# Performance work log

Hardware: AMD Instinct MI355X
Metric: run time of the kernel (lower is better)

## Reference

```python
import jax, jax.numpy as jnp
import numpy as np

N_POINTS = 2_000_000
GRID = 256  # voxel grid resolution (D=H=W), production-scale stand-in for source's 128


def setup_inputs() -> dict:
    key = jax.random.key(0)
    k1, k2, k3 = jax.random.split(key, 3)
    coords = jax.random.uniform(k1, (N_POINTS, 3), dtype=jnp.float32,
                                minval=-0.95, maxval=0.95)
    registration_pred = jax.random.normal(k2, (N_POINTS, 3), dtype=jnp.float32) * 0.02
    registration_gt = jax.random.normal(k3, (N_POINTS, 3), dtype=jnp.float32) * 0.02
    return {"registration_pred": registration_pred,
            "registration_gt": registration_gt,
            "coords": coords}


def _splat(pts, size):
    """Trilinear scatter (adjoint of F.grid_sample, align_corners=False,
    zero padding). pts: [N,3] normalized coords in (x,y,z) order mapping to
    (W,H,D). Splats weight 1 per point. Returns [D,H,W] volume."""
    D = H = W = size
    # grid_sample align_corners=False unnormalization: p = ((g+1)*size - 1)/2
    x = ((pts[:, 0] + 1.0) * W - 1.0) * 0.5
    y = ((pts[:, 1] + 1.0) * H - 1.0) * 0.5
    z = ((pts[:, 2] + 1.0) * D - 1.0) * 0.5
    x0f, y0f, z0f = jnp.floor(x), jnp.floor(y), jnp.floor(z)
    fx, fy, fz = x - x0f, y - y0f, z - z0f  # fractional offsets
    x0, y0, z0 = x0f.astype(jnp.int32), y0f.astype(jnp.int32), z0f.astype(jnp.int32)
    vol = jnp.zeros(D * H * W, dtype=pts.dtype)
    for dz in (0, 1):
        wz = fz if dz else (1.0 - fz)
        for dy in (0, 1):
            wy = fy if dy else (1.0 - fy)
            for dx in (0, 1):
                wx = fx if dx else (1.0 - fx)
                xi, yi, zi = x0 + dx, y0 + dy, z0 + dz
                valid = ((xi >= 0) & (xi < W) & (yi >= 0) & (yi < H)
                         & (zi >= 0) & (zi < D))
                w = jnp.where(valid, wx * wy * wz, 0.0)
                idx = jnp.where(valid, (zi * H + yi) * W + xi, 0)
                vol = vol.at[idx].add(w)
    return vol.reshape(D, H, W)


def reference(registration_pred, registration_gt, coords):
    pred_vol = _splat(coords + registration_pred, GRID)
    gt_vol = _splat(coords + registration_gt, GRID)
    # HuberLoss(reduction='sum', delta=1.0)
    d = pred_vol - gt_vol
    ad = jnp.abs(d)
    return jnp.sum(jnp.where(ad <= 1.0, 0.5 * d * d, ad - 0.5))
```

## Files before the change

kernel.cpp:

```cpp
#include <hip/hip_runtime.h>

#define GRID_RES 256
#define NCELLS 1024
#define NB 1024
#define BCAP 6144
#define CCAP 6144
#define NPT 2

#define W_SCALE 2097152.0f
#define INV_W (1.0f / 2097152.0f)
#define L_SCALE 512.0f
#define INV_L (1.0f / 512.0f)

struct CEv { unsigned pk, xyz; };

__device__ __forceinline__ CEv make_cev(float px, float py, float pz,
                                        unsigned sign) {
    float x = ((px + 1.0f) * (float)GRID_RES - 1.0f) * 0.5f;
    float y = ((py + 1.0f) * (float)GRID_RES - 1.0f) * 0.5f;
    float z = ((pz + 1.0f) * (float)GRID_RES - 1.0f) * 0.5f;
    float xf = floorf(x), yf = floorf(y), zf = floorf(z);
    int x0 = (int)xf, y0 = (int)yf, z0 = (int)zf;
    unsigned qx = (unsigned)((x - xf) * 31.0f + 0.5f);
    unsigned qy = (unsigned)((y - yf) * 31.0f + 0.5f);
    unsigned qz = (unsigned)((z - zf) * 15.0f + 0.5f);
    bool valid = (x0 >= -1) & (x0 <= 255) & (y0 >= -1) & (y0 <= 255) &
                 (z0 >= -1) & (z0 <= 255);
    CEv e;
    e.pk = qx | (qy << 5) | (qz << 10) | (sign << 31);
    e.xyz = valid ? ((unsigned)(x0 + 1) | ((unsigned)(y0 + 1) << 10) |
                     ((unsigned)(z0 + 1) << 20) | (1u << 30))
                  : 0u;
    return e;
}

__device__ __forceinline__ bool ev_flat(const CEv& e, unsigned& cell0,
                                        unsigned& w1base, bool& bx, bool& by,
                                        bool& bz) {
    if (!(e.xyz & (1u << 30))) return false;
    int x0 = (int)(e.xyz & 1023u) - 1;
    int y0 = (int)((e.xyz >> 10) & 1023u) - 1;
    int z0 = (int)((e.xyz >> 20) & 1023u) - 1;
    int xlo = (x0 >= 0) ? (x0 >> 5) : 0;
    int ylo = (y0 >= 0) ? (y0 >> 5) : 0;
    int zlo = (z0 >= 0) ? (z0 >> 4) : 0;
    bx = ((x0 & 31) == 31) & ((unsigned)x0 < 255u);
    by = ((y0 & 31) == 31) & ((unsigned)y0 < 255u);
    bz = ((z0 & 15) == 15) & ((unsigned)z0 < 255u);
    cell0 = ((unsigned)zlo << 6) | ((unsigned)ylo << 3) | (unsigned)xlo;
    unsigned lx0 = (unsigned)(x0 - (xlo << 5) + 1);
    unsigned ly0 = (unsigned)(y0 - (ylo << 5) + 1);
    unsigned lz0 = (unsigned)(z0 - (zlo << 4) + 1);
    w1base = e.pk | (lx0 << 14) | (ly0 << 20) | (lz0 << 26);
    return true;
}

__global__ void init_kernel(unsigned* __restrict__ gCursor,
                            int* __restrict__ lossAcc,
                            unsigned* __restrict__ doneCnt) {
    int t = threadIdx.x;
    gCursor[t] = 0;
    if (t == 0) { lossAcc[0] = 0; doneCnt[0] = 0; }
}

__global__ __launch_bounds__(1024) void bin_kernel(
    const float* __restrict__ pred, const float* __restrict__ gt,
    const float* __restrict__ coords, unsigned* __restrict__ gCursor,
    unsigned* __restrict__ payload, int n) {
    __shared__ unsigned h[NCELLS];
    __shared__ unsigned gAdj[NCELLS];
    __shared__ unsigned short itemCell[BCAP];
    __shared__ unsigned wtot[16];
    __shared__ unsigned totalS;
    __shared__ unsigned pl[BCAP];
    int b = blockIdx.x;
    int t = threadIdx.x;
    h[t] = 0;
    __syncthreads();

    int chunk = (n + NB - 1) / NB;
    int start = b * chunk;
    int end = min(start + chunk, n);
    const float3* c3 = (const float3*)coords;
    const float3* p3 = (const float3*)pred;
    const float3* g3 = (const float3*)gt;

    CEv ev[2 * NPT];
#pragma unroll
    for (int k = 0; k < NPT; ++k) {
        int i = start + t + (k << 10);
        if (i < end) {
            float3 c = c3[i];
            float3 p = p3[i];
            float3 g = g3[i];
            ev[2 * k] = make_cev(c.x + p.x, c.y + p.y, c.z + p.z, 0u);
            ev[2 * k + 1] = make_cev(c.x + g.x, c.y + g.y, c.z + g.z, 1u);
        } else {
            ev[2 * k].xyz = 0;
            ev[2 * k + 1].xyz = 0;
        }
    }

#pragma unroll
    for (int k = 0; k < 2 * NPT; ++k) {
        unsigned cell0, w1base;
        bool bx, by, bz;
        if (ev_flat(ev[k], cell0, w1base, bx, by, bz)) {
#pragma unroll
            for (int q = 0; q < 8; ++q) {
                const int DX = q & 1, DY = (q >> 1) & 1, DZ = q >> 2;
                bool go = (DX ? bx : true) & (DY ? by : true) & (DZ ? bz : true);
                if (go) atomicAdd(&h[cell0 + DX + 8 * DY + 64 * DZ], 1u);
            }
        }
    }
    __syncthreads();

    unsigned x = h[t];
    unsigned xp = x + (x & 1u);
    unsigned incl = xp;
    int lane = t & 63, wid = t >> 6;
#pragma unroll
    for (int off = 1; off < 64; off <<= 1) {
        unsigned y = __shfl_up(incl, off, 64);
        if (lane >= off) incl += y;
    }
    if (lane == 63) wtot[wid] = incl;
    __syncthreads();
    if (t == 0) {
        unsigned r = 0;
#pragma unroll
        for (int w = 0; w < 16; ++w) { unsigned q = wtot[w]; wtot[w] = r; r += q; }
        totalS = r;
    }
    __syncthreads();
    unsigned offE = incl - xp + wtot[wid];
    h[t] = offE;

    if ((x & 1u) && (offE + x) < (unsigned)BCAP) {
        pl[offE + x] = 0u;
        itemCell[offE + x] = (unsigned short)t;
    }

    unsigned gdst = atomicAdd(&gCursor[t], xp);
    gAdj[t] = (unsigned)t * (unsigned)CCAP + gdst - offE;
    __syncthreads();

#pragma unroll
    for (int k = 0; k < 2 * NPT; ++k) {
        unsigned cell0, w1base;
        bool bx, by, bz;
        if (ev_flat(ev[k], cell0, w1base, bx, by, bz)) {
#pragma unroll
            for (int q = 0; q < 8; ++q) {
                const int DX = q & 1, DY = (q >> 1) & 1, DZ = q >> 2;
                bool go = (DX ? bx : true) & (DY ? by : true) & (DZ ? bz : true);
                if (go) {
                    unsigned cell = cell0 + DX + 8 * DY + 64 * DZ;
                    unsigned w1 = w1base - (((unsigned)DX << 19) +
                                            ((unsigned)DY << 25) +
                                            ((unsigned)DZ << 30));
                    unsigned slot = atomicAdd(&h[cell], 1u);
                    if (slot < (unsigned)BCAP) {
                        pl[slot] = w1;
                        itemCell[slot] = (unsigned short)cell;
                    }
                }
            }
        }
    }
    __syncthreads();

    unsigned tot = min(totalS, (unsigned)BCAP);
    unsigned np = tot >> 1;
    const uint2* pl2 = (const uint2*)pl;
    uint2* pay2 = (uint2*)payload;
    for (unsigned j = t; j < np; j += 1024) {
        unsigned cell = itemCell[2 * j];
        unsigned e = gAdj[cell] + 2u * j;
        if (e + 2u <= (cell + 1u) * (unsigned)CCAP) pay2[e >> 1] = pl2[j];
    }
}

__device__ __forceinline__ void accum_item(unsigned p, int* v) {
    float fx = (float)(p & 31u) * (1.0f / 31.0f);
    float fy = (float)((p >> 5) & 31u) * (1.0f / 31.0f);
    float fz = (float)((p >> 10) & 15u) * (1.0f / 15.0f);
    int lx = (int)((p >> 14) & 63u);
    int ly = (int)((p >> 20) & 63u);
    int lz = (int)((p >> 26) & 31u);
    float s = (p >> 31) ? -W_SCALE : W_SCALE;
    float wxs[2] = {1.0f - fx, fx};
    float wys[2] = {1.0f - fy, fy};
    float wzs[2] = {1.0f - fz, fz};
    int xb = lx - 1, yb = ly - 1, zb = lz - 1;
#pragma unroll
    for (int dz = 0; dz < 2; ++dz) {
        int rz = zb + dz;
        if ((unsigned)rz > 15u) continue;
        float wz = s * wzs[dz];
#pragma unroll
        for (int dy = 0; dy < 2; ++dy) {
            int ry = yb + dy;
            if ((unsigned)ry > 31u) continue;
            float wyz = wz * wys[dy];
#pragma unroll
            for (int dx = 0; dx < 2; ++dx) {
                int rx = xb + dx;
                if ((unsigned)rx > 31u) continue;
                int iw = __float2int_rn(wyz * wxs[dx]);
                atomicAdd(&v[(rz << 10) | (ry << 5) | rx], iw);
            }
        }
    }
}

__global__ __launch_bounds__(1024) void accum_kernel(
    const unsigned* __restrict__ payload, const unsigned* __restrict__ gCursor,
    int* __restrict__ lossAcc, unsigned* __restrict__ doneCnt,
    float* __restrict__ out) {
    __shared__ int4 v4s[4096];
    __shared__ float wsum[16];
    int* v = (int*)v4s;
    int c = blockIdx.x;
    int t = threadIdx.x;
    unsigned cnt = min(gCursor[c], (unsigned)CCAP) & ~1u;
    int4 z; z.x = 0; z.y = 0; z.z = 0; z.w = 0;
#pragma unroll
    for (int j = 0; j < 4; ++j) v4s[t + (j << 10)] = z;
    __syncthreads();

    const uint2* p2 = (const uint2*)(payload + (size_t)c * CCAP);
    unsigned n2 = cnt >> 1;
#pragma unroll 2
    for (unsigned i = t; i < n2; i += 1024) {
        uint2 q = p2[i];
        accum_item(q.x, v);
        accum_item(q.y, v);
    }
    __syncthreads();

    int lane = t & 63, wid = t >> 6;
    float acc = 0.0f;
#pragma unroll
    for (int j = 0; j < 4; ++j) {
        int4 q = v4s[t + (j << 10)];
        {
            float d = (float)q.x * INV_W;
            float ad = fabsf(d);
            acc += (ad <= 1.0f) ? 0.5f * d * d : ad - 0.5f;
        }
        {
            float d = (float)q.y * INV_W;
            float ad = fabsf(d);
            acc += (ad <= 1.0f) ? 0.5f * d * d : ad - 0.5f;
        }
        {
            float d = (float)q.z * INV_W;
            float ad = fabsf(d);
            acc += (ad <= 1.0f) ? 0.5f * d * d : ad - 0.5f;
        }
        {
            float d = (float)q.w * INV_W;
            float ad = fabsf(d);
            acc += (ad <= 1.0f) ? 0.5f * d * d : ad - 0.5f;
        }
    }
#pragma unroll
    for (int o = 32; o > 0; o >>= 1) acc += __shfl_down(acc, o, 64);
    if (lane == 0) wsum[wid] = acc;
    __syncthreads();
    if (t == 0) {
        float tsum = 0.0f;
#pragma unroll
        for (int w = 0; w < 16; ++w) tsum += wsum[w];
        atomicAdd(lossAcc, __float2int_rn(tsum * L_SCALE));
        __threadfence();
        unsigned done = atomicAdd(doneCnt, 1u);
        if (done == (unsigned)(NCELLS - 1)) {
            __threadfence();
            int lv = atomicAdd(lossAcc, 0);
            out[0] = (float)lv * INV_L;
        }
    }
}

extern "C" void kernel_launch(void* const* d_in, const int* in_sizes, int n_in,
                              void* d_out, int out_size, void* d_ws, size_t ws_size,
                              hipStream_t stream) {
    const float* reg_pred = (const float*)d_in[0];
    const float* reg_gt   = (const float*)d_in[1];
    const float* coords   = (const float*)d_in[2];
    float* out = (float*)d_out;

    char* ws = (char*)d_ws;
    int* lossAcc = (int*)ws;
    unsigned* doneCnt = (unsigned*)(ws + 64);
    unsigned* gCursor = (unsigned*)(ws + 256);
    unsigned* payload = (unsigned*)(ws + 256 + 4096);

    int n = in_sizes[0] / 3;

    init_kernel<<<1, 1024, 0, stream>>>(gCursor, lossAcc, doneCnt);
    bin_kernel<<<NB, 1024, 0, stream>>>(reg_pred, reg_gt, coords, gCursor,
                                        payload, n);
    accum_kernel<<<NCELLS, 1024, 0, stream>>>(payload, gCursor, lossAcc,
                                              doneCnt, out);
}
```

Baseline: 155.8 us.

## Scatter binned items directly to global payload instead of staging in LDS

The bin kernel no longer stages items in a shared-memory buffer and then copies them out in coalesced uint2 pairs. Each item is written straight to its global slot, computed from the per-cell global offset plus the local atomic slot. This frees about 37KB of LDS per block and drops a barrier and the copy loop, which may raise occupancy. The cost is scattered 4-byte global writes in place of coalesced 8-byte ones. The accum loop unroll also goes from 2 to 4.

New measurement: 177.4 us. 1.14x slower.

```diff
diff --git a/kernel.cpp b/kernel.cpp
--- a/kernel.cpp
+++ b/kernel.cpp
@@ -3,7 +3,6 @@
 #define GRID_RES 256
 #define NCELLS 1024
 #define NB 1024
-#define BCAP 6144
 #define CCAP 6144
 #define NPT 2
 
@@ -69,10 +68,7 @@
     unsigned* __restrict__ payload, int n) {
     __shared__ unsigned h[NCELLS];
     __shared__ unsigned gAdj[NCELLS];
-    __shared__ unsigned short itemCell[BCAP];
     __shared__ unsigned wtot[16];
-    __shared__ unsigned totalS;
-    __shared__ unsigned pl[BCAP];
     int b = blockIdx.x;
     int t = threadIdx.x;
     h[t] = 0;
@@ -131,19 +127,20 @@
         unsigned r = 0;
 #pragma unroll
         for (int w = 0; w < 16; ++w) { unsigned q = wtot[w]; wtot[w] = r; r += q; }
-        totalS = r;
     }
     __syncthreads();
     unsigned offE = incl - xp + wtot[wid];
+
+    unsigned gdst = atomicAdd(&gCursor[t], xp);
+
+    unsigned cellBase = (unsigned)t * (unsigned)CCAP;
+    if (x & 1u) {
+        unsigned d = cellBase + gdst + x;
+        if (d < cellBase + (unsigned)CCAP) payload[d] = 0u;
+    }
+
     h[t] = offE;
-
-    if ((x & 1u) && (offE + x) < (unsigned)BCAP) {
-        pl[offE + x] = 0u;
-        itemCell[offE + x] = (unsigned short)t;
-    }
-
-    unsigned gdst = atomicAdd(&gCursor[t], xp);
-    gAdj[t] = (unsigned)t * (unsigned)CCAP + gdst - offE;
+    gAdj[t] = cellBase + gdst - offE;
     __syncthreads();
 
 #pragma unroll
@@ -161,24 +158,11 @@
                                             ((unsigned)DY << 25) +
                                             ((unsigned)DZ << 30));
                     unsigned slot = atomicAdd(&h[cell], 1u);
-                    if (slot < (unsigned)BCAP) {
-                        pl[slot] = w1;
-                        itemCell[slot] = (unsigned short)cell;
-                    }
+                    unsigned d = gAdj[cell] + slot;
+                    if (d < (cell + 1u) * (unsigned)CCAP) payload[d] = w1;
                 }
             }
         }
-    }
-    __syncthreads();
-
-    unsigned tot = min(totalS, (unsigned)BCAP);
-    unsigned np = tot >> 1;
-    const uint2* pl2 = (const uint2*)pl;
-    uint2* pay2 = (uint2*)payload;
-    for (unsigned j = t; j < np; j += 1024) {
-        unsigned cell = itemCell[2 * j];
-        unsigned e = gAdj[cell] + 2u * j;
-        if (e + 2u <= (cell + 1u) * (unsigned)CCAP) pay2[e >> 1] = pl2[j];
     }
 }
 
@@ -232,7 +216,7 @@
 
     const uint2* p2 = (const uint2*)(payload + (size_t)c * CCAP);
     unsigned n2 = cnt >> 1;
-#pragma unroll 2
+#pragma unroll 4
     for (unsigned i = t; i < n2; i += 1024) {
         uint2 q = p2[i];
         accum_item(q.x, v);
```
